# Performance work log

Hardware: AMD Instinct MI355X
Metric: run time of the kernel (lower is better)

## Reference

```python
import jax, jax.numpy as jnp
import numpy as np

D_MODEL = 256
KSIZE = 16
EPS = 1e-5


def conv1d(x, w, b):
    # x: [B, C, N], w: [O, C, K], SAME padding over node axis
    y = jax.lax.conv_general_dilated(x, w, window_strides=(1,), padding='SAME',
                                     dimension_numbers=('NCH', 'OIH', 'NCH'))
    return y + b[None, :, None]


def layernorm(x, g, b):
    mu = jnp.mean(x, axis=-1, keepdims=True)
    var = jnp.mean(jnp.square(x - mu), axis=-1, keepdims=True)
    return (x - mu) * jax.lax.rsqrt(var + EPS) * g + b


def setup_inputs() -> dict:
    key = jax.random.key(0)
    ks = jax.random.split(key, 16)
    B, N, d, K = 4, 2048, D_MODEL, KSIZE
    conv_scale = 1.0 / np.sqrt(d * K)
    lin_scale = 1.0 / np.sqrt(d)
    return {
        'src': jax.random.normal(ks[0], (B, N, d), jnp.float32),
        'x_lst': jnp.zeros((B, N, N), jnp.float32),
        'adj': jax.random.randint(ks[1], (B, N, N), 0, 2, jnp.int32),
        'dis': jax.random.uniform(ks[2], (B, N, N), jnp.float32),
        'Wq': jax.random.normal(ks[3], (d, d, K), jnp.float32) * conv_scale,
        'bq': jnp.zeros((d,), jnp.float32),
        'Wk': jax.random.normal(ks[4], (d, d, K), jnp.float32) * conv_scale,
        'bk': jnp.zeros((d,), jnp.float32),
        'Wv': jax.random.normal(ks[5], (d, d, K), jnp.float32) * conv_scale,
        'bv': jnp.zeros((d,), jnp.float32),
        'W1': jax.random.normal(ks[6], (d, d), jnp.float32) * lin_scale,
        'b1': jnp.zeros((d,), jnp.float32),
        'W2': jax.random.normal(ks[7], (d, d), jnp.float32) * lin_scale,
        'b2': jnp.zeros((d,), jnp.float32),
        'W3': jax.random.normal(ks[8], (d, d), jnp.float32) * lin_scale,
        'b3': jnp.zeros((d,), jnp.float32),
        'g1': jnp.ones((d,), jnp.float32),
        'be1': jnp.zeros((d,), jnp.float32),
        'g2': jnp.ones((d,), jnp.float32),
        'be2': jnp.zeros((d,), jnp.float32),
    }


def reference(src, x_lst, adj, dis, Wq, bq, Wk, bk, Wv, bv,
              W1, b1, W2, b2, W3, b3, g1, be1, g2, be2):
    # ---- _ga_block: transpose to channel-major, graph attention ----
    x = jnp.swapaxes(src, -2, -1)                      # [B, d, N]
    q = conv1d(x, Wq, bq)                              # [B, d, N]
    k = conv1d(x, Wk, bk)
    v = conv1d(x, Wv, bv)
    scale = 1.0 / jnp.sqrt(jnp.asarray(D_MODEL, src.dtype))
    scores = jnp.einsum('bdn,bdm->bnm', q, k) * scale  # [B, N, N]
    scores = scores - dis                              # distance bias
    scores = jnp.where(adj > 0, scores, jnp.asarray(-1e9, scores.dtype))
    attn = jax.nn.softmax(scores, axis=-1)             # [B, N, N]
    x_lst_new = x_lst + attn                           # accumulated attention state
    out = jnp.einsum('bnm,bdm->bdn', attn, v)          # [B, d, N]
    x1 = jnp.swapaxes(out, -2, -1)                     # [B, N, d] (dropout = identity in eval)
    # ---- residual + norm1 ----
    h = layernorm(src + x1, g1, be1)
    # ---- 3-layer LeakyReLU MLP + residual + norm2 ----
    m = jax.nn.leaky_relu(h @ W1.T + b1)
    m = jax.nn.leaky_relu(m @ W2.T + b2)
    m = m @ W3.T + b3
    h = layernorm(h + m, g2, be2)
    return h, x_lst_new
```

## Files before the change

kernel.cpp:

```cpp
#include <hip/hip_runtime.h>
#include <stdint.h>

typedef _Float16 h16;
typedef _Float16 h8v __attribute__((ext_vector_type(8)));
typedef float    f4v __attribute__((ext_vector_type(4)));
typedef int      i4v __attribute__((ext_vector_type(4)));

#define NBATCH 4
#define NNODE  2048
#define DM     256
#define NPAD   2063
#define QKELEM 2097152
#define PARTN  (8192 * 256)

__device__ __forceinline__ void async16(const void* g, void* l) {
#if __has_builtin(__builtin_amdgcn_global_load_lds)
  __builtin_amdgcn_global_load_lds((__attribute__((address_space(1))) void*)g,
                                   (__attribute__((address_space(3))) void*)l, 16, 0, 0);
#else
  *(f4v*)l = *(const f4v*)g;
#endif
}

__device__ __forceinline__ void gemm_tile(
    const h16* Abase, int astride,
    const h16* Bbase, int bstride,
    h16* As, h16* Bs, f4v acc[4][4], int kiters)
{
  const int tid  = threadIdx.x;
  const int lane = tid & 63;
  const int wv   = tid >> 6;
  const int srow = tid >> 2;
  const int sch  = ((tid & 3) ^ ((tid >> 3) & 3)) * 8;
  const h16* gA0 = Abase + (long)srow * astride + sch;
  const h16* gA1 = Abase + (long)(srow + 64) * astride + sch;
  const h16* gB0 = Bbase + (long)srow * bstride + sch;
  const h16* gB1 = Bbase + (long)(srow + 64) * bstride + sch;
  h16* lA0 = As + tid * 8;
  h16* lA1 = As + 2048 + tid * 8;
  h16* lB0 = Bs + tid * 8;
  h16* lB1 = Bs + 2048 + tid * 8;
  const int swz = ((lane & 15) >> 1) & 3;
  const int qq  = ((lane >> 4) ^ swz) * 8;
  const int amr = ((wv & 1) * 64 + (lane & 15)) * 32 + qq;
  const int bnr = ((wv >> 1) * 64 + (lane & 15)) * 32 + qq;

  for (int kt = 0; kt < kiters; ++kt) {
    const int k0 = kt * 32;
    __syncthreads();
    async16(gA0 + k0, lA0);
    async16(gA1 + k0, lA1);
    async16(gB0 + k0, lB0);
    async16(gB1 + k0, lB1);
    asm volatile("s_waitcnt vmcnt(0)" ::: "memory");
    __syncthreads();
    h8v af[4], bf[4];
#pragma unroll
    for (int i = 0; i < 4; ++i) af[i] = *(const h8v*)(As + amr + i * 512);
#pragma unroll
    for (int j = 0; j < 4; ++j) bf[j] = *(const h8v*)(Bs + bnr + j * 512);
#pragma unroll
    for (int i = 0; i < 4; ++i)
#pragma unroll
      for (int j = 0; j < 4; ++j)
        acc[i][j] = __builtin_amdgcn_mfma_f32_16x16x32_f16(af[i], bf[j], acc[i][j], 0, 0, 0);
  }
}

__device__ __forceinline__ void zero_acc(f4v acc[4][4]) {
#pragma unroll
  for (int i = 0; i < 4; ++i)
#pragma unroll
    for (int j = 0; j < 4; ++j) {
      f4v z = {0.f, 0.f, 0.f, 0.f};
      acc[i][j] = z;
    }
}

__global__ void prep_src_kernel(const float* __restrict__ src, h16* __restrict__ Xpad) {
  int idx = blockIdx.x * 256 + threadIdx.x;
  int c = idx & 255;
  int row = idx >> 8;
  int b = row / NPAD;
  int n = row - b * NPAD;
  float v = 0.f;
  int ns = n - 7;
  if (ns >= 0 && ns < NNODE) v = src[((long)b * NNODE + ns) * DM + c];
  Xpad[idx] = (h16)v;
}

__global__ __launch_bounds__(256) void prep_wconv_kernel(
    const float* __restrict__ Wq, const float* __restrict__ Wk,
    const float* __restrict__ Wv, h16* __restrict__ Wt)
{
  __shared__ float lds[16][257];
  const int w = blockIdx.x >> 8, o = blockIdx.x & 255, tid = threadIdx.x;
  const float* W = (w == 0) ? Wq : (w == 1) ? Wk : Wv;
  const float* base = W + (long)o * 4096;
  f4v r0 = *(const f4v*)(base + tid * 16);
  f4v r1 = *(const f4v*)(base + tid * 16 + 4);
  f4v r2 = *(const f4v*)(base + tid * 16 + 8);
  f4v r3 = *(const f4v*)(base + tid * 16 + 12);
#pragma unroll
  for (int k = 0; k < 4; ++k) {
    lds[k][tid] = r0[k]; lds[4 + k][tid] = r1[k];
    lds[8 + k][tid] = r2[k]; lds[12 + k][tid] = r3[k];
  }
  __syncthreads();
  const int t = tid >> 4, c0 = (tid & 15) * 16;
  h16* out = Wt + ((long)(w * 256 + o)) * 4096 + t * 256 + c0;
  h8v o0, o1;
#pragma unroll
  for (int k = 0; k < 8; ++k) { o0[k] = (h16)lds[t][c0 + k]; o1[k] = (h16)lds[t][c0 + 8 + k]; }
  *(h8v*)out = o0;
  *(h8v*)(out + 8) = o1;
}

__global__ void prep_wlin_kernel(const float* __restrict__ W1, const float* __restrict__ W2,
                                 const float* __restrict__ W3, h16* __restrict__ Wl) {
  int idx = blockIdx.x * 256 + threadIdx.x;
  int w = idx >> 16;
  int rem = idx & 65535;
  const float* W = (w == 0) ? W1 : (w == 1) ? W2 : W3;
  Wl[idx] = (h16)W[rem];
}

__global__ __launch_bounds__(256) void conv_gemm_kernel(
    const h16* __restrict__ Xpad, const h16* __restrict__ Wt,
    h16* __restrict__ Qp, h16* __restrict__ Kp, h16* __restrict__ Vp)
{
  __shared__ __align__(16) h16 As[4096];
  __shared__ __align__(16) h16 Bs[4096];
  const int mt = blockIdx.x, ct = blockIdx.y;
  const int w = blockIdx.z >> 2, ks = blockIdx.z & 3;
  const int m0 = mt * 128;
  const int b = m0 >> 11, n0 = m0 & 2047;
  const h16* Abase = Xpad + ((long)(b * NPAD + n0)) * DM + ks * 1024;
  const h16* Bbase = Wt + (long)w * (256 * 4096) + (long)ct * 128 * 4096 + ks * 1024;
  f4v acc[4][4];
  zero_acc(acc);
  gemm_tile(Abase, DM, Bbase, 4096, As, Bs, acc, 32);

  h16* dst = ((w == 0) ? Qp : (w == 1) ? Kp : Vp) + (long)ks * QKELEM;
  const int lane = threadIdx.x & 63, wv = threadIdx.x >> 6;
  const int rbase = (wv & 1) * 64 + (lane >> 4) * 4;
  const int cbase = (wv >> 1) * 64 + (lane & 15);
#pragma unroll
  for (int j = 0; j < 4; ++j) {
    const int gc = ct * 128 + cbase + j * 16;
#pragma unroll
    for (int i = 0; i < 4; ++i) {
#pragma unroll
      for (int e = 0; e < 4; ++e) {
        const int gr = m0 + rbase + i * 16 + e;
        const h16 v = (h16)acc[i][j][e];
        if (w == 2) {
          const int bb = gr >> 11, n = gr & 2047;
          dst[((long)(bb * 256 + gc)) * 2048 + n] = v;
        } else {
          dst[(long)gr * 256 + gc] = v;
        }
      }
    }
  }
}

__global__ __launch_bounds__(256) void conv_reduce_kernel(
    const h16* __restrict__ Qp, const h16* __restrict__ Kp, const h16* __restrict__ Vp,
    const float* __restrict__ bq, const float* __restrict__ bk, const float* __restrict__ bv,
    h16* __restrict__ Qb, h16* __restrict__ Kb, h16* __restrict__ Vt)
{
  const long gid = (long)blockIdx.x * 256 + threadIdx.x;
  if (gid < 2 * (QKELEM / 8)) {
    const int which = gid >= (QKELEM / 8);
    const long e = (gid - (long)which * (QKELEM / 8)) * 8;
    const h16* P = which ? Kp : Qp;
    const float* bias = which ? bk : bq;
    float s[8] = {0.f, 0.f, 0.f, 0.f, 0.f, 0.f, 0.f, 0.f};
#pragma unroll
    for (int ks = 0; ks < 4; ++ks) {
      h8v p = *(const h8v*)(P + (long)ks * QKELEM + e);
#pragma unroll
      for (int k = 0; k < 8; ++k) s[k] += (float)p[k];
    }
    const int c0 = (int)(e & 255);
    h8v o;
#pragma unroll
    for (int k = 0; k < 8; ++k) o[k] = (h16)(s[k] + bias[c0 + k]);
    *(h8v*)((which ? Kb : Qb) + e) = o;
  } else {
    const long e = (gid - 2 * (QKELEM / 8)) * 8;
    float s[8] = {0.f, 0.f, 0.f, 0.f, 0.f, 0.f, 0.f, 0.f};
#pragma unroll
    for (int ks = 0; ks < 4; ++ks) {
      h8v p = *(const h8v*)(Vp + (long)ks * QKELEM + e);
#pragma unroll
      for (int k = 0; k < 8; ++k) s[k] += (float)p[k];
    }
    const float bias_v = bv[(int)((e >> 11) & 255)];
    h8v o;
#pragma unroll
    for (int k = 0; k < 8; ++k) o[k] = (h16)(s[k] + bias_v);
    *(h8v*)(Vt + e) = o;
  }
}

__global__ __launch_bounds__(256) void scores_gemm_kernel(
    const h16* __restrict__ Q, const h16* __restrict__ Km, h16* __restrict__ Sh)
{
  __shared__ __align__(16) h16 As[4096];
  __shared__ __align__(16) h16 Bs[4096];
  const int nt = blockIdx.x, mt = blockIdx.y, b = blockIdx.z;
  const h16* Abase = Q + ((long)b * NNODE + nt * 128) * 256;
  const h16* Bbase = Km + ((long)b * NNODE + mt * 128) * 256;
  f4v acc[4][4];
  zero_acc(acc);
  gemm_tile(Abase, 256, Bbase, 256, As, Bs, acc, 8);

  const int lane = threadIdx.x & 63, wv = threadIdx.x >> 6;
  const int rbase = (wv & 1) * 64 + (lane >> 4) * 4;
  const int cbase = (wv >> 1) * 64 + (lane & 15);
  h16* Srow = Sh + (long)b * NNODE * NNODE;
#pragma unroll
  for (int i = 0; i < 4; ++i) {
#pragma unroll
    for (int e = 0; e < 4; ++e) {
      const long row = nt * 128 + rbase + i * 16 + e;
#pragma unroll
      for (int j = 0; j < 4; ++j) {
        const int col = mt * 128 + cbase + j * 16;
        Srow[row * 2048 + col] = (h16)(acc[i][j][e] * 0.0625f);
      }
    }
  }
}

__device__ __forceinline__ float wred_max(float v) {
#pragma unroll
  for (int off = 32; off > 0; off >>= 1) v = fmaxf(v, __shfl_xor(v, off, 64));
  return v;
}
__device__ __forceinline__ float wred_sum(float v) {
#pragma unroll
  for (int off = 32; off > 0; off >>= 1) v += __shfl_xor(v, off, 64);
  return v;
}

__global__ __launch_bounds__(256) void softmax_kernel(
    h16* __restrict__ Sh, const float* __restrict__ dis, const int* __restrict__ adj,
    const float* __restrict__ x_lst, float* __restrict__ out_x)
{
  const int r = blockIdx.x;
  const long ro = (long)r * 2048;
  const int tid = threadIdx.x, lane = tid & 63, wv = tid >> 6;
  const int j0 = tid * 8;
  __shared__ float wmax[4], wsum[4];

  h8v sv = *(const h8v*)(Sh + ro + j0);
  f4v d0 = *(const f4v*)(dis + ro + j0);
  f4v d1 = *(const f4v*)(dis + ro + j0 + 4);
  i4v a0 = *(const i4v*)(adj + ro + j0);
  i4v a1 = *(const i4v*)(adj + ro + j0 + 4);

  float s[8];
#pragma unroll
  for (int k = 0; k < 4; ++k) s[k]     = (a0[k] > 0) ? ((float)sv[k]     - d0[k]) : -1e9f;
#pragma unroll
  for (int k = 0; k < 4; ++k) s[k + 4] = (a1[k] > 0) ? ((float)sv[k + 4] - d1[k]) : -1e9f;

  float m = s[0];
#pragma unroll
  for (int k = 1; k < 8; ++k) m = fmaxf(m, s[k]);
  m = wred_max(m);
  if (lane == 0) wmax[wv] = m;
  __syncthreads();
  m = fmaxf(fmaxf(wmax[0], wmax[1]), fmaxf(wmax[2], wmax[3]));

  float p[8], ls = 0.f;
#pragma unroll
  for (int k = 0; k < 8; ++k) { p[k] = __expf(s[k] - m); ls += p[k]; }
  ls = wred_sum(ls);
  if (lane == 0) wsum[wv] = ls;
  __syncthreads();
  const float inv = 1.0f / (wsum[0] + wsum[1] + wsum[2] + wsum[3]);

  f4v x0 = *(const f4v*)(x_lst + ro + j0);
  f4v x1 = *(const f4v*)(x_lst + ro + j0 + 4);
  f4v o0, o1;
  h8v pv;
#pragma unroll
  for (int k = 0; k < 4; ++k) {
    const float a = p[k] * inv, bq = p[k + 4] * inv;
    o0[k] = x0[k] + a; o1[k] = x1[k] + bq;
    pv[k] = (h16)a; pv[k + 4] = (h16)bq;
  }
  *(f4v*)(out_x + ro + j0) = o0;
  *(f4v*)(out_x + ro + j0 + 4) = o1;
  *(h8v*)(Sh + ro + j0) = pv;
}

__global__ __launch_bounds__(256) void av_gemm_kernel(
    const h16* __restrict__ Attn, const h16* __restrict__ Vt, float* __restrict__ X1p)
{
  __shared__ __align__(16) h16 As[4096];
  __shared__ __align__(16) h16 Bs[4096];
  const int nt = blockIdx.x, b = blockIdx.z;
  const int ct = blockIdx.y & 1, ks = blockIdx.y >> 1;
  const h16* Abase = Attn + ((long)b * NNODE + nt * 128) * 2048 + ks * 1024;
  const h16* Bbase = Vt + ((long)b * 256 + ct * 128) * 2048 + ks * 1024;
  f4v acc[4][4];
  zero_acc(acc);
  gemm_tile(Abase, 2048, Bbase, 2048, As, Bs, acc, 32);

  const int lane = threadIdx.x & 63, wv = threadIdx.x >> 6;
  const int rbase = (wv & 1) * 64 + (lane >> 4) * 4;
  const int cbase = (wv >> 1) * 64 + (lane & 15);
  float* dst = X1p + (long)ks * PARTN;
#pragma unroll
  for (int i = 0; i < 4; ++i) {
#pragma unroll
    for (int e = 0; e < 4; ++e) {
      const long row = (long)b * NNODE + nt * 128 + rbase + i * 16 + e;
#pragma unroll
      for (int j = 0; j < 4; ++j) {
        const int col = ct * 128 + cbase + j * 16;
        dst[row * 256 + col] = acc[i][j][e];
      }
    }
  }
}

__global__ __launch_bounds__(256) void mlp_gemm_kernel(
    const h16* __restrict__ A, const h16* __restrict__ W, const float* __restrict__ bias,
    h16* __restrict__ outH, float* __restrict__ outF)
{
  __shared__ __align__(16) h16 As[4096];
  __shared__ __align__(16) h16 Bs[4096];
  const int mt = blockIdx.x, ct = blockIdx.y;
  const h16* Abase = A + (long)mt * 128 * 256;
  const h16* Bbase = W + (long)ct * 128 * 256;
  f4v acc[4][4];
  zero_acc(acc);
  gemm_tile(Abase, 256, Bbase, 256, As, Bs, acc, 8);

  const int lane = threadIdx.x & 63, wv = threadIdx.x >> 6;
  const int rbase = (wv & 1) * 64 + (lane >> 4) * 4;
  const int cbase = (wv >> 1) * 64 + (lane & 15);
#pragma unroll
  for (int j = 0; j < 4; ++j) {
    const int gc = ct * 128 + cbase + j * 16;
    const float bias_v = bias[gc];
#pragma unroll
    for (int i = 0; i < 4; ++i) {
#pragma unroll
      for (int e = 0; e < 4; ++e) {
        const long gr = (long)mt * 128 + rbase + i * 16 + e;
        float v = acc[i][j][e] + bias_v;
        if (outH) {
          v = (v >= 0.f) ? v : 0.01f * v;
          outH[gr * 256 + gc] = (h16)v;
        } else {
          outF[gr * 256 + gc] = v;
        }
      }
    }
  }
}

__global__ __launch_bounds__(256) void ln_kernel(
    const float* __restrict__ X, const float* __restrict__ Y, const float* __restrict__ Y2,
    const float* __restrict__ g, const float* __restrict__ bb,
    float* __restrict__ outF, h16* __restrict__ outH)
{
  const int wv = threadIdx.x >> 6, lane = threadIdx.x & 63;
  const long r = (long)blockIdx.x * 4 + wv;
  const long off = r * 256 + lane * 4;
  f4v x = *(const f4v*)(X + off);
  f4v y = *(const f4v*)(Y + off);
  if (Y2) {
    f4v y2 = *(const f4v*)(Y2 + off);
#pragma unroll
    for (int k = 0; k < 4; ++k) y[k] += y2[k];
  }
  float v[4];
  float sum = 0.f, sq = 0.f;
#pragma unroll
  for (int k = 0; k < 4; ++k) { v[k] = x[k] + y[k]; sum += v[k]; sq += v[k] * v[k]; }
  sum = wred_sum(sum);
  sq  = wred_sum(sq);
  const float mu = sum * (1.0f / 256.0f);
  const float var = sq * (1.0f / 256.0f) - mu * mu;
  const float rs = rsqrtf(var + 1e-5f);
  f4v gg = *(const f4v*)(g + lane * 4);
  f4v be = *(const f4v*)(bb + lane * 4);
  f4v o;
#pragma unroll
  for (int k = 0; k < 4; ++k) o[k] = (v[k] - mu) * rs * gg[k] + be[k];
  if (outF) *(f4v*)(outF + off) = o;
  if (outH) {
    _Float16 hv[4];
#pragma unroll
    for (int k = 0; k < 4; ++k) hv[k] = (h16)o[k];
    *(ulong1*)(outH + off) = *(ulong1*)hv;
  }
}

extern "C" void kernel_launch(void* const* d_in, const int* in_sizes, int n_in,
                              void* d_out, int out_size, void* d_ws, size_t ws_size,
                              hipStream_t stream)
{
  const float* src  = (const float*)d_in[0];
  const float* xlst = (const float*)d_in[1];
  const int*   adj  = (const int*)d_in[2];
  const float* dis  = (const float*)d_in[3];
  const float* Wq   = (const float*)d_in[4];
  const float* bq   = (const float*)d_in[5];
  const float* Wk   = (const float*)d_in[6];
  const float* bk   = (const float*)d_in[7];
  const float* Wv   = (const float*)d_in[8];
  const float* bvp  = (const float*)d_in[9];
  const float* W1   = (const float*)d_in[10];
  const float* b1   = (const float*)d_in[11];
  const float* W2   = (const float*)d_in[12];
  const float* b2   = (const float*)d_in[13];
  const float* W3   = (const float*)d_in[14];
  const float* b3   = (const float*)d_in[15];
  const float* g1   = (const float*)d_in[16];
  const float* be1  = (const float*)d_in[17];
  const float* g2   = (const float*)d_in[18];
  const float* be2  = (const float*)d_in[19];
  (void)in_sizes; (void)n_in; (void)out_size; (void)ws_size;

  char* ws = (char*)d_ws;
  size_t off = 0;
  auto alloc = [&](size_t bytes) -> void* {
    void* p = ws + off;
    off += (bytes + 1023) & ~(size_t)1023;
    return p;
  };
  h16*   Xpad = (h16*)  alloc((size_t)NBATCH * NPAD * DM * 2);
  h16*   Wt   = (h16*)  alloc((size_t)3 * 256 * 4096 * 2);
  h16*   Wl   = (h16*)  alloc((size_t)3 * 256 * 256 * 2);
  h16*   Qb   = (h16*)  alloc((size_t)QKELEM * 2);
  h16*   Kb   = (h16*)  alloc((size_t)QKELEM * 2);
  h16*   Vt   = (h16*)  alloc((size_t)QKELEM * 2);
  char*  R    = (char*) alloc((size_t)71400 * 1024);
  h16*   Qp   = (h16*)R;
  h16*   Kp   = (h16*)(R + (size_t)4 * QKELEM * 2);
  h16*   Vp   = (h16*)(R + (size_t)8 * QKELEM * 2);
  h16*   Sh   = (h16*)R;
  float* X1p  = (float*)(R + (size_t)16 * QKELEM);
  float* H    = (float*)(R + (size_t)16 * QKELEM + (size_t)2 * PARTN * 4);
  h16*   H16  = (h16*)((char*)H + (size_t)PARTN * 4);
  h16*   M1   = (h16*)((char*)H16 + (size_t)PARTN * 2);
  h16*   M2   = (h16*)((char*)M1 + (size_t)PARTN * 2);
  float* M3   = X1p;

  float* out_h = (float*)d_out;
  float* out_x = out_h + (size_t)NBATCH * NNODE * DM;

  prep_src_kernel<<<(NBATCH * NPAD * DM) / 256, 256, 0, stream>>>(src, Xpad);
  prep_wconv_kernel<<<3 * 256, 256, 0, stream>>>(Wq, Wk, Wv, Wt);
  prep_wlin_kernel<<<(3 * 256 * 256) / 256, 256, 0, stream>>>(W1, W2, W3, Wl);

  conv_gemm_kernel<<<dim3(64, 2, 12), 256, 0, stream>>>(Xpad, Wt, Qp, Kp, Vp);
  conv_reduce_kernel<<<3 * (QKELEM / 8) / 256, 256, 0, stream>>>(
      Qp, Kp, Vp, bq, bk, bvp, Qb, Kb, Vt);
  scores_gemm_kernel<<<dim3(16, 16, 4), 256, 0, stream>>>(Qb, Kb, Sh);
  softmax_kernel<<<NBATCH * NNODE, 256, 0, stream>>>(Sh, dis, adj, xlst, out_x);
  av_gemm_kernel<<<dim3(16, 4, 4), 256, 0, stream>>>(Sh, Vt, X1p);
  ln_kernel<<<(NBATCH * NNODE) / 4, 256, 0, stream>>>(src, X1p, X1p + PARTN, g1, be1, H, H16);
  mlp_gemm_kernel<<<dim3(64, 2), 256, 0, stream>>>(H16, Wl, b1, M1, nullptr);
  mlp_gemm_kernel<<<dim3(64, 2), 256, 0, stream>>>(M1, Wl + 65536, b2, M2, nullptr);
  mlp_gemm_kernel<<<dim3(64, 2), 256, 0, stream>>>(M2, Wl + 2 * 65536, b3, nullptr, M3);
  ln_kernel<<<(NBATCH * NNODE) / 4, 256, 0, stream>>>(H, M3, nullptr, g2, be2, out_h, nullptr);
}
```

Measured before the change: 462.8 us.

## Fuse MLP layers with final layernorm, merge prep kernels, store AV partials in fp16

Merges the three preprocessing kernels into one launch, and fuses the three MLP GEMMs plus the second layernorm into a single kernel. That kernel keeps 32-row activation tiles in LDS across layers, which removes the intermediate global round trips. The AV GEMM split-K partials are now written as fp16 instead of fp32, halving their traffic, and the layernorm reads them as fp16. Risks include lower precision in the partial sums and low MFMA utilisation from small 32-row tiles with synchronous weight loads.

```diff
diff --git a/kernel.cpp b/kernel.cpp
--- a/kernel.cpp
+++ b/kernel.cpp
@@ -2,6 +2,7 @@
 #include <stdint.h>
 
 typedef _Float16 h16;
+typedef _Float16 h4v __attribute__((ext_vector_type(4)));
 typedef _Float16 h8v __attribute__((ext_vector_type(8)));
 typedef float    f4v __attribute__((ext_vector_type(4)));
 typedef int      i4v __attribute__((ext_vector_type(4)));
@@ -77,52 +78,54 @@
     }
 }
 
-__global__ void prep_src_kernel(const float* __restrict__ src, h16* __restrict__ Xpad) {
-  int idx = blockIdx.x * 256 + threadIdx.x;
-  int c = idx & 255;
-  int row = idx >> 8;
-  int b = row / NPAD;
-  int n = row - b * NPAD;
-  float v = 0.f;
-  int ns = n - 7;
-  if (ns >= 0 && ns < NNODE) v = src[((long)b * NNODE + ns) * DM + c];
-  Xpad[idx] = (h16)v;
-}
-
-__global__ __launch_bounds__(256) void prep_wconv_kernel(
-    const float* __restrict__ Wq, const float* __restrict__ Wk,
-    const float* __restrict__ Wv, h16* __restrict__ Wt)
-{
-  __shared__ float lds[16][257];
-  const int w = blockIdx.x >> 8, o = blockIdx.x & 255, tid = threadIdx.x;
-  const float* W = (w == 0) ? Wq : (w == 1) ? Wk : Wv;
-  const float* base = W + (long)o * 4096;
-  f4v r0 = *(const f4v*)(base + tid * 16);
-  f4v r1 = *(const f4v*)(base + tid * 16 + 4);
-  f4v r2 = *(const f4v*)(base + tid * 16 + 8);
-  f4v r3 = *(const f4v*)(base + tid * 16 + 12);
-#pragma unroll
-  for (int k = 0; k < 4; ++k) {
-    lds[k][tid] = r0[k]; lds[4 + k][tid] = r1[k];
-    lds[8 + k][tid] = r2[k]; lds[12 + k][tid] = r3[k];
-  }
-  __syncthreads();
-  const int t = tid >> 4, c0 = (tid & 15) * 16;
-  h16* out = Wt + ((long)(w * 256 + o)) * 4096 + t * 256 + c0;
-  h8v o0, o1;
-#pragma unroll
-  for (int k = 0; k < 8; ++k) { o0[k] = (h16)lds[t][c0 + k]; o1[k] = (h16)lds[t][c0 + 8 + k]; }
-  *(h8v*)out = o0;
-  *(h8v*)(out + 8) = o1;
-}
-
-__global__ void prep_wlin_kernel(const float* __restrict__ W1, const float* __restrict__ W2,
-                                 const float* __restrict__ W3, h16* __restrict__ Wl) {
-  int idx = blockIdx.x * 256 + threadIdx.x;
-  int w = idx >> 16;
-  int rem = idx & 65535;
-  const float* W = (w == 0) ? W1 : (w == 1) ? W2 : W3;
-  Wl[idx] = (h16)W[rem];
+#define NSRC_BLK 8252
+__global__ __launch_bounds__(256) void prep_all_kernel(
+    const float* __restrict__ src,
+    const float* __restrict__ Wq, const float* __restrict__ Wk, const float* __restrict__ Wv,
+    const float* __restrict__ W1, const float* __restrict__ W2, const float* __restrict__ W3,
+    h16* __restrict__ Xpad, h16* __restrict__ Wt, h16* __restrict__ Wl)
+{
+  __shared__ float plds[16][257];
+  const int bi = blockIdx.x, tid = threadIdx.x;
+  if (bi < NSRC_BLK) {
+    int idx = bi * 256 + tid;
+    int c = idx & 255;
+    int row = idx >> 8;
+    int b = row / NPAD;
+    int n = row - b * NPAD;
+    float v = 0.f;
+    int ns = n - 7;
+    if (ns >= 0 && ns < NNODE) v = src[((long)b * NNODE + ns) * DM + c];
+    Xpad[idx] = (h16)v;
+  } else if (bi < NSRC_BLK + 768) {
+    const int q = bi - NSRC_BLK;
+    const int w = q >> 8, o = q & 255;
+    const float* W = (w == 0) ? Wq : (w == 1) ? Wk : Wv;
+    const float* base = W + (long)o * 4096;
+    f4v r0 = *(const f4v*)(base + tid * 16);
+    f4v r1 = *(const f4v*)(base + tid * 16 + 4);
+    f4v r2 = *(const f4v*)(base + tid * 16 + 8);
+    f4v r3 = *(const f4v*)(base + tid * 16 + 12);
+#pragma unroll
+    for (int k = 0; k < 4; ++k) {
+      plds[k][tid] = r0[k]; plds[4 + k][tid] = r1[k];
+      plds[8 + k][tid] = r2[k]; plds[12 + k][tid] = r3[k];
+    }
+    __syncthreads();
+    const int t = tid >> 4, c0 = (tid & 15) * 16;
+    h16* out = Wt + ((long)(w * 256 + o)) * 4096 + t * 256 + c0;
+    h8v o0, o1;
+#pragma unroll
+    for (int k = 0; k < 8; ++k) { o0[k] = (h16)plds[t][c0 + k]; o1[k] = (h16)plds[t][c0 + 8 + k]; }
+    *(h8v*)out = o0;
+    *(h8v*)(out + 8) = o1;
+  } else {
+    int idx = (bi - NSRC_BLK - 768) * 256 + tid;
+    int w = idx >> 16;
+    int rem = idx & 65535;
+    const float* W = (w == 0) ? W1 : (w == 1) ? W2 : W3;
+    Wl[idx] = (h16)W[rem];
+  }
 }
 
 __global__ __launch_bounds__(256) void conv_gemm_kernel(
@@ -300,7 +303,7 @@
 }
 
 __global__ __launch_bounds__(256) void av_gemm_kernel(
-    const h16* __restrict__ Attn, const h16* __restrict__ Vt, float* __restrict__ X1p)
+    const h16* __restrict__ Attn, const h16* __restrict__ Vt, h16* __restrict__ X1p)
 {
   __shared__ __align__(16) h16 As[4096];
   __shared__ __align__(16) h16 Bs[4096];
@@ -315,7 +318,7 @@
   const int lane = threadIdx.x & 63, wv = threadIdx.x >> 6;
   const int rbase = (wv & 1) * 64 + (lane >> 4) * 4;
   const int cbase = (wv >> 1) * 64 + (lane & 15);
-  float* dst = X1p + (long)ks * PARTN;
+  h16* dst = X1p + (long)ks * PARTN;
 #pragma unroll
   for (int i = 0; i < 4; ++i) {
 #pragma unroll
@@ -324,51 +327,14 @@
 #pragma unroll
       for (int j = 0; j < 4; ++j) {
         const int col = ct * 128 + cbase + j * 16;
-        dst[row * 256 + col] = acc[i][j][e];
+        dst[row * 256 + col] = (h16)acc[i][j][e];
       }
     }
   }
 }
 
-__global__ __launch_bounds__(256) void mlp_gemm_kernel(
-    const h16* __restrict__ A, const h16* __restrict__ W, const float* __restrict__ bias,
-    h16* __restrict__ outH, float* __restrict__ outF)
-{
-  __shared__ __align__(16) h16 As[4096];
-  __shared__ __align__(16) h16 Bs[4096];
-  const int mt = blockIdx.x, ct = blockIdx.y;
-  const h16* Abase = A + (long)mt * 128 * 256;
-  const h16* Bbase = W + (long)ct * 128 * 256;
-  f4v acc[4][4];
-  zero_acc(acc);
-  gemm_tile(Abase, 256, Bbase, 256, As, Bs, acc, 8);
-
-  const int lane = threadIdx.x & 63, wv = threadIdx.x >> 6;
-  const int rbase = (wv & 1) * 64 + (lane >> 4) * 4;
-  const int cbase = (wv >> 1) * 64 + (lane & 15);
-#pragma unroll
-  for (int j = 0; j < 4; ++j) {
-    const int gc = ct * 128 + cbase + j * 16;
-    const float bias_v = bias[gc];
-#pragma unroll
-    for (int i = 0; i < 4; ++i) {
-#pragma unroll
-      for (int e = 0; e < 4; ++e) {
-        const long gr = (long)mt * 128 + rbase + i * 16 + e;
-        float v = acc[i][j][e] + bias_v;
-        if (outH) {
-          v = (v >= 0.f) ? v : 0.01f * v;
-          outH[gr * 256 + gc] = (h16)v;
-        } else {
-          outF[gr * 256 + gc] = v;
-        }
-      }
-    }
-  }
-}
-
-__global__ __launch_bounds__(256) void ln_kernel(
-    const float* __restrict__ X, const float* __restrict__ Y, const float* __restrict__ Y2,
+__global__ __launch_bounds__(256) void ln1_kernel(
+    const float* __restrict__ X, const h16* __restrict__ Y, const h16* __restrict__ Y2,
     const float* __restrict__ g, const float* __restrict__ bb,
     float* __restrict__ outF, h16* __restrict__ outH)
 {
@@ -376,16 +342,15 @@
   const long r = (long)blockIdx.x * 4 + wv;
   const long off = r * 256 + lane * 4;
   f4v x = *(const f4v*)(X + off);
-  f4v y = *(const f4v*)(Y + off);
-  if (Y2) {
-    f4v y2 = *(const f4v*)(Y2 + off);
-#pragma unroll
-    for (int k = 0; k < 4; ++k) y[k] += y2[k];
-  }
+  h4v y = *(const h4v*)(Y + off);
+  h4v y2 = *(const h4v*)(Y2 + off);
   float v[4];
   float sum = 0.f, sq = 0.f;
 #pragma unroll
-  for (int k = 0; k < 4; ++k) { v[k] = x[k] + y[k]; sum += v[k]; sq += v[k] * v[k]; }
+  for (int k = 0; k < 4; ++k) {
+    v[k] = x[k] + (float)y[k] + (float)y2[k];
+    sum += v[k]; sq += v[k] * v[k];
+  }
   sum = wred_sum(sum);
   sq  = wred_sum(sq);
   const float mu = sum * (1.0f / 256.0f);
@@ -396,12 +361,122 @@
   f4v o;
 #pragma unroll
   for (int k = 0; k < 4; ++k) o[k] = (v[k] - mu) * rs * gg[k] + be[k];
-  if (outF) *(f4v*)(outF + off) = o;
-  if (outH) {
-    _Float16 hv[4];
-#pragma unroll
-    for (int k = 0; k < 4; ++k) hv[k] = (h16)o[k];
-    *(ulong1*)(outH + off) = *(ulong1*)hv;
+  *(f4v*)(outF + off) = o;
+  h4v hv;
+#pragma unroll
+  for (int k = 0; k < 4; ++k) hv[k] = (h16)o[k];
+  *(h4v*)(outH + off) = hv;
+}
+
+__global__ __launch_bounds__(256) void mlp_fused_kernel(
+    const h16* __restrict__ H16, const float* __restrict__ Hf,
+    const h16* __restrict__ Wl,
+    const float* __restrict__ b1, const float* __restrict__ b2, const float* __restrict__ b3,
+    const float* __restrict__ g2, const float* __restrict__ be2,
+    float* __restrict__ out_h)
+{
+  __shared__ h16 Xa[32][264];
+  __shared__ h16 Xb[32][264];
+  __shared__ __align__(16) h16 Bs[8192];
+  const int tid = threadIdx.x, lane = tid & 63, wv = tid >> 6;
+  const int m0 = blockIdx.x * 32;
+
+  {
+    const int r = tid >> 3, cq = (tid & 7) * 32;
+    const h16* s = H16 + (long)(m0 + r) * 256 + cq;
+#pragma unroll
+    for (int k = 0; k < 4; ++k)
+      *(h8v*)&Xa[r][cq + k * 8] = *(const h8v*)(s + k * 8);
+  }
+
+  const int srow = tid >> 2;
+  const int sch  = ((tid & 3) ^ ((tid >> 3) & 3)) * 8;
+  h16* lB = Bs + tid * 8;
+  const int quad = lane >> 4;
+  const float* biases[3] = {b1, b2, b3};
+
+  for (int layer = 0; layer < 3; ++layer) {
+    const h16* W = Wl + layer * 65536;
+    const h16 (*Xi)[264] = (layer == 1) ? (const h16(*)[264])Xb : (const h16(*)[264])Xa;
+    h16 (*Xo)[264] = (layer == 1) ? Xa : Xb;
+    f4v acc[2][4];
+#pragma unroll
+    for (int i = 0; i < 2; ++i)
+#pragma unroll
+      for (int j = 0; j < 4; ++j) { f4v z = {0.f,0.f,0.f,0.f}; acc[i][j] = z; }
+
+    for (int kt = 0; kt < 8; ++kt) {
+      __syncthreads();
+      const h16* gB = W + (long)srow * 256 + kt * 32 + sch;
+      async16(gB, lB);
+      async16(gB + 64 * 256, lB + 64 * 32);
+      async16(gB + 128 * 256, lB + 128 * 32);
+      async16(gB + 192 * 256, lB + 192 * 32);
+      asm volatile("s_waitcnt vmcnt(0)" ::: "memory");
+      __syncthreads();
+      h8v af[2], bf[4];
+#pragma unroll
+      for (int i = 0; i < 2; ++i)
+        af[i] = *(const h8v*)&Xi[i * 16 + (lane & 15)][kt * 32 + quad * 8];
+#pragma unroll
+      for (int j = 0; j < 4; ++j) {
+        const int n = wv * 64 + j * 16 + (lane & 15);
+        const int q = (quad ^ ((n >> 1) & 3)) * 8;
+        bf[j] = *(const h8v*)(Bs + n * 32 + q);
+      }
+#pragma unroll
+      for (int i = 0; i < 2; ++i)
+#pragma unroll
+        for (int j = 0; j < 4; ++j)
+          acc[i][j] = __builtin_amdgcn_mfma_f32_16x16x32_f16(af[i], bf[j], acc[i][j], 0, 0, 0);
+    }
+    const int rb = quad * 4;
+    const int cb = wv * 64 + (lane & 15);
+    const float* bias = biases[layer];
+    const bool leaky = (layer < 2);
+#pragma unroll
+    for (int j = 0; j < 4; ++j) {
+      const int col = cb + j * 16;
+      const float bv = bias[col];
+#pragma unroll
+      for (int i = 0; i < 2; ++i)
+#pragma unroll
+        for (int e = 0; e < 4; ++e) {
+          float v = acc[i][j][e] + bv;
+          if (leaky) v = (v >= 0.f) ? v : 0.01f * v;
+          Xo[i * 16 + rb + e][col] = (h16)v;
+        }
+    }
+  }
+  __syncthreads();
+
+  const int r = tid >> 3, c0 = (tid & 7) * 32;
+  const float* hrow = Hf + (long)(m0 + r) * 256 + c0;
+  float v[32];
+  float s = 0.f, sq = 0.f;
+#pragma unroll
+  for (int k8 = 0; k8 < 8; ++k8) {
+    f4v h4 = *(const f4v*)(hrow + k8 * 4);
+#pragma unroll
+    for (int e = 0; e < 4; ++e) {
+      float t = (float)Xb[r][c0 + k8 * 4 + e] + h4[e];
+      v[k8 * 4 + e] = t; s += t; sq += t * t;
+    }
+  }
+#pragma unroll
+  for (int off = 1; off < 8; off <<= 1) { s += __shfl_xor(s, off, 64); sq += __shfl_xor(sq, off, 64); }
+  const float mu = s * (1.0f / 256.0f);
+  const float var = sq * (1.0f / 256.0f) - mu * mu;
+  const float rs = rsqrtf(var + 1e-5f);
+  float* orow = out_h + (long)(m0 + r) * 256 + c0;
+#pragma unroll
+  for (int k8 = 0; k8 < 8; ++k8) {
+    f4v gg = *(const f4v*)(g2 + c0 + k8 * 4);
+    f4v be = *(const f4v*)(be2 + c0 + k8 * 4);
+    f4v o;
+#pragma unroll
+    for (int e = 0; e < 4; ++e) o[e] = (v[k8 * 4 + e] - mu) * rs * gg[e] + be[e];
+    *(f4v*)(orow + k8 * 4) = o;
   }
 }
 
@@ -444,34 +519,27 @@
   h16*   Qb   = (h16*)  alloc((size_t)QKELEM * 2);
   h16*   Kb   = (h16*)  alloc((size_t)QKELEM * 2);
   h16*   Vt   = (h16*)  alloc((size_t)QKELEM * 2);
-  char*  R    = (char*) alloc((size_t)71400 * 1024);
+  char*  R    = (char*) alloc((size_t)66000 * 1024);
   h16*   Qp   = (h16*)R;
   h16*   Kp   = (h16*)(R + (size_t)4 * QKELEM * 2);
   h16*   Vp   = (h16*)(R + (size_t)8 * QKELEM * 2);
   h16*   Sh   = (h16*)R;
-  float* X1p  = (float*)(R + (size_t)16 * QKELEM);
-  float* H    = (float*)(R + (size_t)16 * QKELEM + (size_t)2 * PARTN * 4);
+  h16*   X1p  = Vp;
+  float* H    = (float*)(R + (size_t)12 * QKELEM * 2);
   h16*   H16  = (h16*)((char*)H + (size_t)PARTN * 4);
-  h16*   M1   = (h16*)((char*)H16 + (size_t)PARTN * 2);
-  h16*   M2   = (h16*)((char*)M1 + (size_t)PARTN * 2);
-  float* M3   = X1p;
 
   float* out_h = (float*)d_out;
   float* out_x = out_h + (size_t)NBATCH * NNODE * DM;
 
-  prep_src_kernel<<<(NBATCH * NPAD * DM) / 256, 256, 0, stream>>>(src, Xpad);
-  prep_wconv_kernel<<<3 * 256, 256, 0, stream>>>(Wq, Wk, Wv, Wt);
-  prep_wlin_kernel<<<(3 * 256 * 256) / 256, 256, 0, stream>>>(W1, W2, W3, Wl);
-
+  prep_all_kernel<<<NSRC_BLK + 768 + 768, 256, 0, stream>>>(
+      src, Wq, Wk, Wv, W1, W2, W3, Xpad, Wt, Wl);
   conv_gemm_kernel<<<dim3(64, 2, 12), 256, 0, stream>>>(Xpad, Wt, Qp, Kp, Vp);
   conv_reduce_kernel<<<3 * (QKELEM / 8) / 256, 256, 0, stream>>>(
       Qp, Kp, Vp, bq, bk, bvp, Qb, Kb, Vt);
   scores_gemm_kernel<<<dim3(16, 16, 4), 256, 0, stream>>>(Qb, Kb, Sh);
   softmax_kernel<<<NBATCH * NNODE, 256, 0, stream>>>(Sh, dis, adj, xlst, out_x);
   av_gemm_kernel<<<dim3(16, 4, 4), 256, 0, stream>>>(Sh, Vt, X1p);
-  ln_kernel<<<(NBATCH * NNODE) / 4, 256, 0, stream>>>(src, X1p, X1p + PARTN, g1, be1, H, H16);
-  mlp_gemm_kernel<<<dim3(64, 2), 256, 0, stream>>>(H16, Wl, b1, M1, nullptr);
-  mlp_gemm_kernel<<<dim3(64, 2), 256, 0, stream>>>(M1, Wl + 65536, b2, M2, nullptr);
-  mlp_gemm_kernel<<<dim3(64, 2), 256, 0, stream>>>(M2, Wl + 2 * 65536, b3, nullptr, M3);
-  ln_kernel<<<(NBATCH * NNODE) / 4, 256, 0, stream>>>(H, M3, nullptr, g2, be2, out_h, nullptr);
-}
+  ln1_kernel<<<(NBATCH * NNODE) / 4, 256, 0, stream>>>(src, X1p, X1p + PARTN, g1, be1, H, H16);
+  mlp_fused_kernel<<<NBATCH * NNODE / 32, 256, 0, stream>>>(
+      H16, H, Wl, b1, b2, b3, g2, be2, out_h);
+}
```

Result: faster. 445.0 us (-3.8%).
